# Optimization experiments

Measured on AMD Instinct MI355X. Metric: run time of the kernel, lower is better.

The kernel has to match this reference:

```python
import jax, jax.numpy as jnp
import numpy as np

RADIUS = 1.3
COARSE = 64
FINE = 2
N_ATOMS = 64
SH_DIM = 9
DATA_DIM = SH_DIM * 3 + 1  # 28
N_INTRS = COARSE * 3 * 2 * FINE  # 768
STEP = (RADIUS * 2.0 / COARSE / FINE) / 2.0
BATCH = 1024


def sh_basis(d):
    # real spherical harmonics basis, degree 2 (9 coeffs), on normalized dirs
    d = d / jnp.linalg.norm(d, axis=-1, keepdims=True)
    x, y, z = d[..., 0], d[..., 1], d[..., 2]
    C0 = 0.28209479177387814
    C1 = 0.4886025119029199
    C20, C21, C22, C23, C24 = (1.0925484305920792, -1.0925484305920792,
                               0.31539156525252005, -1.0925484305920792,
                               0.5462742152960396)
    return jnp.stack([
        C0 * jnp.ones_like(x), -C1 * y, C1 * z, -C1 * x,
        C20 * x * y, C21 * y * z, C22 * (2.0 * z * z - x * x - y * y),
        C23 * x * z, C24 * (x * x - y * y)
    ], axis=-1)


def dict_interp(grid, atoms, pts):
    # l2_interp_v2: coarse-voxel dictionary coeffs x trilinear fine-atom interp
    # pts: [P,3] in [0,1)
    P = pts.shape[0]
    pc = pts * COARSE
    c = jnp.clip(jnp.floor(pc), 0, COARSE - 1).astype(jnp.int32)
    local = pc - c.astype(pts.dtype)  # position inside coarse voxel, [0,1)
    clin = (c[:, 0] * COARSE + c[:, 1]) * COARSE + c[:, 2]
    coeff = grid[clin]                              # [P, A]
    # project dictionary coeffs through atoms for every fine cell: [P, FINE^3, D]
    proj = jnp.einsum('pa,fad->pfd', coeff, atoms)
    u = local * FINE - 0.5
    f = jnp.floor(u)
    t = u - f
    i0 = jnp.clip(f, 0, FINE - 1).astype(jnp.int32)
    i1 = jnp.clip(f + 1.0, 0, FINE - 1).astype(jnp.int32)
    idx = jnp.stack([i0, i1], axis=-1)              # [P,3,2]
    w = jnp.stack([1.0 - t, t], axis=-1)            # [P,3,2]
    rows = jnp.arange(P)
    out = jnp.zeros((P, DATA_DIM), dtype=pts.dtype)
    for kx in (0, 1):
        for ky in (0, 1):
            for kz in (0, 1):
                lin = (idx[:, 0, kx] * FINE + idx[:, 1, ky]) * FINE + idx[:, 2, kz]
                wgt = w[:, 0, kx] * w[:, 1, ky] * w[:, 2, kz]
                out = out + wgt[:, None] * proj[rows, lin]
    return out


def _forward(rays_o, rays_d, grid, atoms):
    dt = rays_o.dtype
    # ---- sample_proposal (no grad) ----
    off_pos = (RADIUS - rays_o) / rays_d
    off_neg = (-RADIUS - rays_o) / rays_d
    start = jnp.max(jnp.minimum(off_pos, off_neg), axis=-1, keepdims=True)
    intersections = jax.lax.stop_gradient(
        start + jnp.arange(N_INTRS, dtype=dt)[None, :] * STEP)  # [B, 768]
    tr = intersections[:, :-1]  # [B, 767]
    pts = rays_o[:, None, :] + tr[..., None] * rays_d[:, None, :]  # [B,n,3]
    mask = jnp.all((pts > -RADIUS) & (pts < RADIUS), axis=-1)      # [B,n]
    pts = jax.lax.stop_gradient(pts)
    B, n = tr.shape
    # normalized coords in [0,1); masked-out points are clipped then zeroed later
    p = jnp.clip((pts + RADIUS) / (2.0 * RADIUS), 0.0, 1.0 - 1e-6).reshape(-1, 3)
    data = dict_interp(grid, atoms, p).reshape(B, n, DATA_DIM)
    # masked_scatter of sigma <=> dense compute + where(mask, ., 0)
    sigma = jnp.where(mask, jax.nn.relu(data[..., -1]), 0.0)
    dists = (intersections[:, 1:] - intersections[:, :-1]) * \
        jnp.linalg.norm(rays_d, axis=-1, keepdims=True)
    alpha = 1.0 - jnp.exp(-sigma * dists)
    trans = jnp.cumprod(1.0 - alpha + 1e-10, axis=-1)
    trans = jnp.concatenate([jnp.ones_like(trans[:, :1]), trans[:, :-1]], axis=-1)
    abs_light = alpha * trans  # per-sample weights
    sh_mult = sh_basis(rays_d)                      # [B, 9]
    sh = data[..., :-1].reshape(B, n, 3, SH_DIM)
    rgb_samp = jnp.einsum('bnck,bk->bnc', sh, sh_mult)
    rgb_samp = jax.nn.sigmoid(jnp.where(mask[..., None], rgb_samp, 0.0))
    comp = jnp.sum(abs_light[..., None] * rgb_samp, axis=1)  # [B,3]
    acc = jnp.sum(abs_light, axis=1)
    rgb = comp + (1.0 - acc)[:, None]  # white background
    depth = jnp.sum(abs_light * tr, axis=1)
    return rgb, alpha, depth


def setup_inputs():
    key = jax.random.key(0)
    k0, k1, k2, k3 = jax.random.split(key, 4)
    o = jax.random.normal(k0, (BATCH, 3), dtype=jnp.float32)
    o = o / jnp.linalg.norm(o, axis=-1, keepdims=True) * 2.5
    d = -o + 0.3 * jax.random.normal(k1, (BATCH, 3), dtype=jnp.float32)
    d = d / jnp.linalg.norm(d, axis=-1, keepdims=True)
    grid = 0.01 * jax.random.normal(k2, (COARSE ** 3, N_ATOMS), dtype=jnp.float32)
    atoms_sh = jax.random.uniform(k3, (FINE ** 3, N_ATOMS, DATA_DIM - 1), dtype=jnp.float32)
    atoms = jnp.concatenate(
        [atoms_sh, jnp.full((FINE ** 3, N_ATOMS, 1), 0.01, dtype=jnp.float32)], axis=-1)
    return {"rays_o": o, "rays_d": d, "grid": grid, "atoms": atoms, "grid_id": 0}


def reference(rays_o, rays_d, grid, atoms, grid_id):
    # grid_id selects among num_scenes grids; num_scenes=1 so grid is pre-selected
    return _forward(rays_o, rays_d, grid, atoms)
```

## Files before the change

kernel.cpp:

```cpp
#include <hip/hip_runtime.h>
#include <hip/hip_bf16.h>

#define RADIUS_F 1.3f
#define NSAMP 767
#define STEPF 0.01015625f
#define BATCH 1024

typedef __attribute__((ext_vector_type(8))) short short8;
typedef __attribute__((ext_vector_type(4))) float floatx4;
typedef __fp16 fp16x2 __attribute__((ext_vector_type(2)));

static __device__ __forceinline__ unsigned pkbf(float a, float b) {
    union { __hip_bfloat162 h; unsigned u; } cvt;
    cvt.h = __float22bfloat162_rn(make_float2(a, b));
    return cvt.u;
}
static __device__ __forceinline__ unsigned pkh(float a, float b) {
    union { fp16x2 h; unsigned u; } c;
    c.h = __builtin_amdgcn_cvt_pkrtz(a, b);
    return c.u;
}
static __device__ __forceinline__ float2 uph(unsigned u) {
    union { unsigned u; fp16x2 h; } c; c.u = u;
    return make_float2((float)c.h.x, (float)c.h.y);
}
static __device__ __forceinline__ float bfx(unsigned short u) {
    union { unsigned u; float f; } c; c.u = ((unsigned)u) << 16; return c.f;
}

static __device__ __forceinline__ float coset4_sum(float p) {
    int q4 = __builtin_amdgcn_update_dpp(0, __float_as_int(p), 0x124, 0xf, 0xf, true);
    p = p + __int_as_float(q4);
    int q8 = __builtin_amdgcn_update_dpp(0, __float_as_int(p), 0x128, 0xf, 0xf, true);
    return p + __int_as_float(q8);
}

__launch_bounds__(512, 8)
__global__ void plenoxels_fwd(const float* __restrict__ rays_o,
                              const float* __restrict__ rays_d,
                              const float* __restrict__ grid,
                              const float* __restrict__ atoms,
                              float* __restrict__ out)
{
    __shared__ __align__(16) __hip_bfloat16 BpL[32 * 64];
    __shared__ unsigned WpU[768 * 5];
    __shared__ __align__(16) __hip_bfloat16 pL[768 * 4];
    __shared__ float wprodL[8];
    __shared__ float partL[8][5];

    const int tid  = threadIdx.x;
    const int ray  = blockIdx.x;
    const int lane = tid & 63;
    const int w    = tid >> 6;
    const int m    = lane & 15;
    const int quad = lane >> 4;

    const float ox = rays_o[ray * 3 + 0], oy = rays_o[ray * 3 + 1], oz = rays_o[ray * 3 + 2];
    const float dx = rays_d[ray * 3 + 0], dy = rays_d[ray * 3 + 1], dz = rays_d[ray * 3 + 2];

    float start;
    {
        float a0 = (RADIUS_F - ox) / dx, b0 = (-RADIUS_F - ox) / dx;
        float a1 = (RADIUS_F - oy) / dy, b1 = (-RADIUS_F - oy) / dy;
        float a2 = (RADIUS_F - oz) / dz, b2 = (-RADIUS_F - oz) / dz;
        start = fmaxf(fminf(a0, b0), fmaxf(fminf(a1, b1), fminf(a2, b2)));
    }
    const float dnorm = sqrtf(dx * dx + dy * dy + dz * dz);
    const float dist = STEPF * dnorm;

    auto geom = [&](int s) -> int {
        float tr = start + (float)s * STEPF;
        float px = ox + tr * dx, py = oy + tr * dy, pz = oz + tr * dz;
        int mask = (px > -RADIUS_F) & (px < RADIUS_F) &
                   (py > -RADIUS_F) & (py < RADIUS_F) &
                   (pz > -RADIUS_F) & (pz < RADIUS_F) & (s < NSAMP);
        float maskf = mask ? 1.f : 0.f;
        const float sc = 1.0f / (2.0f * RADIUS_F);
        float qx = fminf(fmaxf((px + RADIUS_F) * sc, 0.f), 1.0f - 1e-6f);
        float qy = fminf(fmaxf((py + RADIUS_F) * sc, 0.f), 1.0f - 1e-6f);
        float qz = fminf(fmaxf((pz + RADIUS_F) * sc, 0.f), 1.0f - 1e-6f);
        float pcx = qx * 64.f, pcy = qy * 64.f, pcz = qz * 64.f;
        float cx = fminf(floorf(pcx), 63.f);
        float cy = fminf(floorf(pcy), 63.f);
        float cz = fminf(floorf(pcz), 63.f);
        float lx = pcx - cx, ly = pcy - cy, lz = pcz - cz;
        int clin = (((int)cx * 64) + (int)cy) * 64 + (int)cz;
        float xw0, xw1, yw0, yw1, zw0, zw1;
        {
            float u = lx * 2.f - 0.5f, fF = floorf(u), t = u - fF;
            xw0 = (fF < 0.f) ? 1.f : ((fF > 0.f) ? 0.f : 1.f - t);
            xw1 = (fF < 0.f) ? 0.f : ((fF > 0.f) ? 1.f : t);
        }
        {
            float u = ly * 2.f - 0.5f, fF = floorf(u), t = u - fF;
            yw0 = (fF < 0.f) ? 1.f : ((fF > 0.f) ? 0.f : 1.f - t);
            yw1 = (fF < 0.f) ? 0.f : ((fF > 0.f) ? 1.f : t);
        }
        {
            float u = lz * 2.f - 0.5f, fF = floorf(u), t = u - fF;
            zw0 = (fF < 0.f) ? 1.f : ((fF > 0.f) ? 0.f : 1.f - t);
            zw1 = (fF < 0.f) ? 0.f : ((fF > 0.f) ? 1.f : t);
        }
        xw0 *= maskf; xw1 *= maskf;
        float g0 = yw0 * zw0, g1 = yw0 * zw1, g2 = yw1 * zw0, g3 = yw1 * zw1;
        unsigned* wr = &WpU[s * 5];
        wr[0] = pkh(xw0 * g0, xw1 * g0);
        wr[1] = pkh(xw0 * g1, xw1 * g1);
        wr[2] = pkh(xw0 * g2, xw1 * g2);
        wr[3] = pkh(xw0 * g3, xw1 * g3);
        return clin;
    };

    int clinA = geom(w * 96 + lane);
    int clinB = 0;
    if (lane < 32) clinB = geom(w * 96 + 64 + lane);

    const float4* g4 = (const float4*)grid;
    float4 cv0, cv1, cv2, cv3;
    {
        int clinC = __shfl(clinA, m, 64);
        const float4* gp = g4 + (clinC << 4) + (quad << 2);
        cv0 = gp[0]; cv1 = gp[1]; cv2 = gp[2]; cv3 = gp[3];
    }

    {
        float shm[9];
        float inv = 1.0f / dnorm;
        float nx = dx * inv, ny = dy * inv, nz = dz * inv;
        shm[0] = 0.28209479177387814f;
        shm[1] = -0.4886025119029199f * ny;
        shm[2] = 0.4886025119029199f * nz;
        shm[3] = -0.4886025119029199f * nx;
        shm[4] = 1.0925484305920792f * nx * ny;
        shm[5] = -1.0925484305920792f * ny * nz;
        shm[6] = 0.31539156525252005f * (2.f * nz * nz - nx * nx - ny * ny);
        shm[7] = -1.0925484305920792f * nx * nz;
        shm[8] = 0.5462742152960396f * (nx * nx - ny * ny);

        const float* base = atoms + tid * 28;
        float4 v0 = *(const float4*)(base);
        float4 v1 = *(const float4*)(base + 4);
        float4 v2 = *(const float4*)(base + 8);
        float4 v3 = *(const float4*)(base + 12);
        float4 v4 = *(const float4*)(base + 16);
        float4 v5 = *(const float4*)(base + 20);
        float4 v6 = *(const float4*)(base + 24);

        float s0 = v0.x*shm[0] + v0.y*shm[1] + v0.z*shm[2] + v0.w*shm[3]
                 + v1.x*shm[4] + v1.y*shm[5] + v1.z*shm[6] + v1.w*shm[7] + v2.x*shm[8];
        float s1 = v2.y*shm[0] + v2.z*shm[1] + v2.w*shm[2] + v3.x*shm[3]
                 + v3.y*shm[4] + v3.z*shm[5] + v3.w*shm[6] + v4.x*shm[7] + v4.y*shm[8];
        float s2 = v4.z*shm[0] + v4.w*shm[1] + v5.x*shm[2] + v5.y*shm[3]
                 + v5.z*shm[4] + v5.w*shm[5] + v6.x*shm[6] + v6.y*shm[7] + v6.z*shm[8];

        int f = tid >> 6, a = tid & 63;
        int cb = (f << 2) << 6;
        BpL[cb + a]        = __float2bfloat16(s0);
        BpL[cb + 64 + a]   = __float2bfloat16(s1);
        BpL[cb + 128 + a]  = __float2bfloat16(s2);
        BpL[cb + 192 + a]  = __float2bfloat16(v6.w);
    }
    __syncthreads();

    short8 bq00, bq01, bq10, bq11;
    {
        const short* bs = (const short*)BpL;
        const short* p0 = bs + m * 64 + (quad << 4);
        bq00 = *(const short8*)(p0);
        bq01 = *(const short8*)(p0 + 8);
        const short* p1 = bs + (16 + m) * 64 + (quad << 4);
        bq10 = *(const short8*)(p1);
        bq11 = *(const short8*)(p1 + 8);
    }

    float* out_rgb   = out;
    float* out_alpha = out + BATCH * 3;
    float* out_depth = out + BATCH * 3 + BATCH * NSAMP;
    const int f0 = m >> 2;

    #pragma unroll
    for (int t = 0; t < 6; ++t) {
        union { unsigned u[4]; short8 s; } a0, a1;
        a0.u[0] = pkbf(cv0.x, cv0.y); a0.u[1] = pkbf(cv0.z, cv0.w);
        a0.u[2] = pkbf(cv1.x, cv1.y); a0.u[3] = pkbf(cv1.z, cv1.w);
        a1.u[0] = pkbf(cv2.x, cv2.y); a1.u[1] = pkbf(cv2.z, cv2.w);
        a1.u[2] = pkbf(cv3.x, cv3.y); a1.u[3] = pkbf(cv3.z, cv3.w);

        if (t < 5) {
            int tn = t + 1;
            int clinC = (tn < 4) ? __shfl(clinA, (tn << 4) + m, 64)
                                 : __shfl(clinB, ((tn - 4) << 4) + m, 64);
            const float4* gp = g4 + (clinC << 4) + (quad << 2);
            cv0 = gp[0]; cv1 = gp[1]; cv2 = gp[2]; cv3 = gp[3];
        }

        floatx4 acc0 = {0.f, 0.f, 0.f, 0.f};
        floatx4 acc1 = {0.f, 0.f, 0.f, 0.f};
        acc0 = __builtin_amdgcn_mfma_f32_16x16x32_bf16(a0.s, bq00, acc0, 0, 0, 0);
        acc0 = __builtin_amdgcn_mfma_f32_16x16x32_bf16(a1.s, bq01, acc0, 0, 0, 0);
        acc1 = __builtin_amdgcn_mfma_f32_16x16x32_bf16(a0.s, bq10, acc1, 0, 0, 0);
        acc1 = __builtin_amdgcn_mfma_f32_16x16x32_bf16(a1.s, bq11, acc1, 0, 0, 0);

        #pragma unroll
        for (int r = 0; r < 4; ++r) {
            int s = w * 96 + (t << 4) + (quad << 2) + r;
            float2 wab = uph(WpU[s * 5 + f0]);
            float p = wab.x * acc0[r] + wab.y * acc1[r];
            p = coset4_sum(p);
            if (m < 4) pL[(s << 2) + m] = __float2bfloat16(p);
        }
    }

    __syncthreads();

    {
        const bool act = (tid < 384);
        const int s0 = tid * 2;
        float a0 = 0.f, a1 = 0.f;
        float r0 = 0.f, g0 = 0.f, b0 = 0.f, r1 = 0.f, g1 = 0.f, b1 = 0.f;
        if (act) {
            short8 pv = *(const short8*)&pL[s0 << 2];
            a0 = 1.f - __expf(-fmaxf(bfx((unsigned short)pv[3]), 0.f) * dist);
            a1 = 1.f - __expf(-fmaxf(bfx((unsigned short)pv[7]), 0.f) * dist);
            r0 = 1.f / (1.f + __expf(-bfx((unsigned short)pv[0])));
            g0 = 1.f / (1.f + __expf(-bfx((unsigned short)pv[1])));
            b0 = 1.f / (1.f + __expf(-bfx((unsigned short)pv[2])));
            r1 = 1.f / (1.f + __expf(-bfx((unsigned short)pv[4])));
            g1 = 1.f / (1.f + __expf(-bfx((unsigned short)pv[5])));
            b1 = 1.f / (1.f + __expf(-bfx((unsigned short)pv[6])));
            out_alpha[ray * NSAMP + s0] = a0;
            if (s0 + 1 < NSAMP) out_alpha[ray * NSAMP + s0 + 1] = a1;
        }
        float pr = (1.f - a0 + 1e-10f) * (1.f - a1 + 1e-10f);

        float incl = pr;
        #pragma unroll
        for (int off = 1; off < 64; off <<= 1) {
            float v = __shfl_up(incl, off, 64);
            if (lane >= off) incl *= v;
        }
        if (lane == 63) wprodL[w] = incl;
        __syncthreads();

        float base = 1.f;
        #pragma unroll
        for (int ww = 0; ww < 5; ++ww)
            if (w > ww) base *= wprodL[ww];
        float excl = __shfl_up(incl, 1, 64);
        if (lane == 0) excl = 1.f;
        float trans = base * excl;

        float c0 = 0.f, c1 = 0.f, c2 = 0.f, accw = 0.f, dep = 0.f;
        if (act) {
            float w0 = a0 * trans;
            c0 += w0 * r0; c1 += w0 * g0; c2 += w0 * b0;
            accw += w0;
            dep += w0 * (start + (float)s0 * STEPF);
            trans *= (1.f - a0 + 1e-10f);
            float w1 = a1 * trans;
            c0 += w1 * r1; c1 += w1 * g1; c2 += w1 * b1;
            accw += w1;
            dep += w1 * (start + (float)(s0 + 1) * STEPF);
        }
        #pragma unroll
        for (int off = 1; off < 64; off <<= 1) {
            c0   += __shfl_xor(c0, off, 64);
            c1   += __shfl_xor(c1, off, 64);
            c2   += __shfl_xor(c2, off, 64);
            accw += __shfl_xor(accw, off, 64);
            dep  += __shfl_xor(dep, off, 64);
        }
        if (lane == 0) {
            partL[w][0] = c0; partL[w][1] = c1; partL[w][2] = c2;
            partL[w][3] = accw; partL[w][4] = dep;
        }
        __syncthreads();
        if (tid == 0) {
            float C0 = 0.f, C1 = 0.f, C2 = 0.f, AC = 0.f, DP = 0.f;
            #pragma unroll
            for (int ww = 0; ww < 6; ++ww) {
                C0 += partL[ww][0]; C1 += partL[ww][1]; C2 += partL[ww][2];
                AC += partL[ww][3]; DP += partL[ww][4];
            }
            float bg = 1.f - AC;
            out_rgb[ray * 3 + 0] = C0 + bg;
            out_rgb[ray * 3 + 1] = C1 + bg;
            out_rgb[ray * 3 + 2] = C2 + bg;
            out_depth[ray] = DP;
        }
    }
}

extern "C" void kernel_launch(void* const* d_in, const int* in_sizes, int n_in,
                              void* d_out, int out_size, void* d_ws, size_t ws_size,
                              hipStream_t stream) {
    const float* rays_o = (const float*)d_in[0];
    const float* rays_d = (const float*)d_in[1];
    const float* grid   = (const float*)d_in[2];
    const float* atoms  = (const float*)d_in[3];
    float* out = (float*)d_out;
    hipLaunchKernelGGL(plenoxels_fwd, dim3(BATCH), dim3(512), 0, stream,
                       rays_o, rays_d, grid, atoms, out);
}
```

Measured before the change: 114.3 us.

## Skip samples outside the box and fuse activations into the MFMA epilogue

Computes each ray's box exit time and the number of samples that can be inside the box. It then distributes only those samples across the waves, so grid gathers and MFMA tiles run only for that range. Samples beyond the range are written as zero alpha, which matches the masked reference. Sigmoid and alpha activations move into the MFMA epilogue and are stored as fp32. Interpolation weights get a transposed layout for vector loads, and the B staging buffer is padded to reduce LDS bank conflicts. In exchange, the unrolled fixed loop becomes a runtime-bounded one, and the trip count varies across blocks.

```diff
diff --git a/kernel.cpp b/kernel.cpp
--- a/kernel.cpp
+++ b/kernel.cpp
@@ -8,6 +8,7 @@
 
 typedef __attribute__((ext_vector_type(8))) short short8;
 typedef __attribute__((ext_vector_type(4))) float floatx4;
+typedef __attribute__((ext_vector_type(4))) unsigned uintx4;
 typedef __fp16 fp16x2 __attribute__((ext_vector_type(2)));
 
 static __device__ __forceinline__ unsigned pkbf(float a, float b) {
@@ -23,9 +24,6 @@
 static __device__ __forceinline__ float2 uph(unsigned u) {
     union { unsigned u; fp16x2 h; } c; c.u = u;
     return make_float2((float)c.h.x, (float)c.h.y);
-}
-static __device__ __forceinline__ float bfx(unsigned short u) {
-    union { unsigned u; float f; } c; c.u = ((unsigned)u) << 16; return c.f;
 }
 
 static __device__ __forceinline__ float coset4_sum(float p) {
@@ -42,9 +40,9 @@
                               const float* __restrict__ atoms,
                               float* __restrict__ out)
 {
-    __shared__ __align__(16) __hip_bfloat16 BpL[32 * 64];
-    __shared__ unsigned WpU[768 * 5];
-    __shared__ __align__(16) __hip_bfloat16 pL[768 * 4];
+    __shared__ __align__(16) __hip_bfloat16 BpL[32 * 72];
+    __shared__ __align__(16) unsigned WtU[4 * 776];
+    __shared__ __align__(16) float pAct[768 * 4];
     __shared__ float wprodL[8];
     __shared__ float partL[8][5];
 
@@ -58,15 +56,25 @@
     const float ox = rays_o[ray * 3 + 0], oy = rays_o[ray * 3 + 1], oz = rays_o[ray * 3 + 2];
     const float dx = rays_d[ray * 3 + 0], dy = rays_d[ray * 3 + 1], dz = rays_d[ray * 3 + 2];
 
-    float start;
+    float start, exitT;
     {
         float a0 = (RADIUS_F - ox) / dx, b0 = (-RADIUS_F - ox) / dx;
         float a1 = (RADIUS_F - oy) / dy, b1 = (-RADIUS_F - oy) / dy;
         float a2 = (RADIUS_F - oz) / dz, b2 = (-RADIUS_F - oz) / dz;
         start = fmaxf(fminf(a0, b0), fmaxf(fminf(a1, b1), fminf(a2, b2)));
+        exitT = fminf(fmaxf(a0, b0), fminf(fmaxf(a1, b1), fmaxf(a2, b2)));
     }
     const float dnorm = sqrtf(dx * dx + dy * dy + dz * dz);
     const float dist = STEPF * dnorm;
+
+    int nAct;
+    {
+        float span = (exitT - start) / STEPF;
+        if (span >= 0.f) nAct = (span < 765.f) ? ((int)span + 2) : NSAMP;
+        else             nAct = (span < 0.f) ? 0 : NSAMP;
+    }
+    const int seg = ((nAct + 127) >> 7) << 4;
+    const int nT  = seg >> 4;
 
     auto geom = [&](int s) -> int {
         float tr = start + (float)s * STEPF;
@@ -103,21 +111,20 @@
         }
         xw0 *= maskf; xw1 *= maskf;
         float g0 = yw0 * zw0, g1 = yw0 * zw1, g2 = yw1 * zw0, g3 = yw1 * zw1;
-        unsigned* wr = &WpU[s * 5];
-        wr[0] = pkh(xw0 * g0, xw1 * g0);
-        wr[1] = pkh(xw0 * g1, xw1 * g1);
-        wr[2] = pkh(xw0 * g2, xw1 * g2);
-        wr[3] = pkh(xw0 * g3, xw1 * g3);
+        WtU[       s] = pkh(xw0 * g0, xw1 * g0);
+        WtU[ 776 + s] = pkh(xw0 * g1, xw1 * g1);
+        WtU[1552 + s] = pkh(xw0 * g2, xw1 * g2);
+        WtU[2328 + s] = pkh(xw0 * g3, xw1 * g3);
         return clin;
     };
 
-    int clinA = geom(w * 96 + lane);
-    int clinB = 0;
-    if (lane < 32) clinB = geom(w * 96 + 64 + lane);
+    int clinA = 0, clinB = 0;
+    if (lane < seg)      clinA = geom(w * seg + lane);
+    if (lane + 64 < seg) clinB = geom(w * seg + 64 + lane);
 
     const float4* g4 = (const float4*)grid;
     float4 cv0, cv1, cv2, cv3;
-    {
+    if (nT > 0) {
         int clinC = __shfl(clinA, m, 64);
         const float4* gp = g4 + (clinC << 4) + (quad << 2);
         cv0 = gp[0]; cv1 = gp[1]; cv2 = gp[2]; cv3 = gp[3];
@@ -154,21 +161,21 @@
                  + v5.z*shm[4] + v5.w*shm[5] + v6.x*shm[6] + v6.y*shm[7] + v6.z*shm[8];
 
         int f = tid >> 6, a = tid & 63;
-        int cb = (f << 2) << 6;
-        BpL[cb + a]        = __float2bfloat16(s0);
-        BpL[cb + 64 + a]   = __float2bfloat16(s1);
-        BpL[cb + 128 + a]  = __float2bfloat16(s2);
-        BpL[cb + 192 + a]  = __float2bfloat16(v6.w);
+        int cb = (f << 2) * 72 + a;
+        BpL[cb]        = __float2bfloat16(s0);
+        BpL[cb + 72]   = __float2bfloat16(s1);
+        BpL[cb + 144]  = __float2bfloat16(s2);
+        BpL[cb + 216]  = __float2bfloat16(v6.w);
     }
     __syncthreads();
 
     short8 bq00, bq01, bq10, bq11;
     {
         const short* bs = (const short*)BpL;
-        const short* p0 = bs + m * 64 + (quad << 4);
+        const short* p0 = bs + m * 72 + (quad << 4);
         bq00 = *(const short8*)(p0);
         bq01 = *(const short8*)(p0 + 8);
-        const short* p1 = bs + (16 + m) * 64 + (quad << 4);
+        const short* p1 = bs + (16 + m) * 72 + (quad << 4);
         bq10 = *(const short8*)(p1);
         bq11 = *(const short8*)(p1 + 8);
     }
@@ -178,56 +185,61 @@
     float* out_depth = out + BATCH * 3 + BATCH * NSAMP;
     const int f0 = m >> 2;
 
-    #pragma unroll
-    for (int t = 0; t < 6; ++t) {
-        union { unsigned u[4]; short8 s; } a0, a1;
-        a0.u[0] = pkbf(cv0.x, cv0.y); a0.u[1] = pkbf(cv0.z, cv0.w);
-        a0.u[2] = pkbf(cv1.x, cv1.y); a0.u[3] = pkbf(cv1.z, cv1.w);
-        a1.u[0] = pkbf(cv2.x, cv2.y); a1.u[1] = pkbf(cv2.z, cv2.w);
-        a1.u[2] = pkbf(cv3.x, cv3.y); a1.u[3] = pkbf(cv3.z, cv3.w);
-
-        if (t < 5) {
-            int tn = t + 1;
-            int clinC = (tn < 4) ? __shfl(clinA, (tn << 4) + m, 64)
-                                 : __shfl(clinB, ((tn - 4) << 4) + m, 64);
+    for (int t = 0; t < nT; ++t) {
+        union { unsigned u[4]; short8 s; } a0p, a1p;
+        a0p.u[0] = pkbf(cv0.x, cv0.y); a0p.u[1] = pkbf(cv0.z, cv0.w);
+        a0p.u[2] = pkbf(cv1.x, cv1.y); a0p.u[3] = pkbf(cv1.z, cv1.w);
+        a1p.u[0] = pkbf(cv2.x, cv2.y); a1p.u[1] = pkbf(cv2.z, cv2.w);
+        a1p.u[2] = pkbf(cv3.x, cv3.y); a1p.u[3] = pkbf(cv3.z, cv3.w);
+
+        if (t + 1 < nT) {
+            int idx = ((t + 1) << 4) + m;
+            int clinC = (idx < 64) ? __shfl(clinA, idx, 64)
+                                   : __shfl(clinB, idx - 64, 64);
             const float4* gp = g4 + (clinC << 4) + (quad << 2);
             cv0 = gp[0]; cv1 = gp[1]; cv2 = gp[2]; cv3 = gp[3];
         }
 
         floatx4 acc0 = {0.f, 0.f, 0.f, 0.f};
         floatx4 acc1 = {0.f, 0.f, 0.f, 0.f};
-        acc0 = __builtin_amdgcn_mfma_f32_16x16x32_bf16(a0.s, bq00, acc0, 0, 0, 0);
-        acc0 = __builtin_amdgcn_mfma_f32_16x16x32_bf16(a1.s, bq01, acc0, 0, 0, 0);
-        acc1 = __builtin_amdgcn_mfma_f32_16x16x32_bf16(a0.s, bq10, acc1, 0, 0, 0);
-        acc1 = __builtin_amdgcn_mfma_f32_16x16x32_bf16(a1.s, bq11, acc1, 0, 0, 0);
-
+        acc0 = __builtin_amdgcn_mfma_f32_16x16x32_bf16(a0p.s, bq00, acc0, 0, 0, 0);
+        acc0 = __builtin_amdgcn_mfma_f32_16x16x32_bf16(a1p.s, bq01, acc0, 0, 0, 0);
+        acc1 = __builtin_amdgcn_mfma_f32_16x16x32_bf16(a0p.s, bq10, acc1, 0, 0, 0);
+        acc1 = __builtin_amdgcn_mfma_f32_16x16x32_bf16(a1p.s, bq11, acc1, 0, 0, 0);
+
+        int sb = w * seg + (t << 4) + (quad << 2);
+        union { uintx4 v; unsigned u[4]; } wt;
+        wt.v = *(const uintx4*)&WtU[f0 * 776 + sb];
         #pragma unroll
         for (int r = 0; r < 4; ++r) {
-            int s = w * 96 + (t << 4) + (quad << 2) + r;
-            float2 wab = uph(WpU[s * 5 + f0]);
+            float2 wab = uph(wt.u[r]);
             float p = wab.x * acc0[r] + wab.y * acc1[r];
             p = coset4_sum(p);
-            if (m < 4) pL[(s << 2) + m] = __float2bfloat16(p);
+            if (m < 4) {
+                float e = __expf((m == 3) ? (-fmaxf(p, 0.f) * dist) : -p);
+                float v = (m == 3) ? (1.f - e) : (1.f / (1.f + e));
+                pAct[((sb + r) << 2) + m] = v;
+            }
         }
     }
 
     __syncthreads();
 
     {
+        const int sLim = seg << 3;
         const bool act = (tid < 384);
         const int s0 = tid * 2;
         float a0 = 0.f, a1 = 0.f;
-        float r0 = 0.f, g0 = 0.f, b0 = 0.f, r1 = 0.f, g1 = 0.f, b1 = 0.f;
+        float r0 = 0.f, g0c = 0.f, b0c = 0.f, r1 = 0.f, g1c = 0.f, b1c = 0.f;
         if (act) {
-            short8 pv = *(const short8*)&pL[s0 << 2];
-            a0 = 1.f - __expf(-fmaxf(bfx((unsigned short)pv[3]), 0.f) * dist);
-            a1 = 1.f - __expf(-fmaxf(bfx((unsigned short)pv[7]), 0.f) * dist);
-            r0 = 1.f / (1.f + __expf(-bfx((unsigned short)pv[0])));
-            g0 = 1.f / (1.f + __expf(-bfx((unsigned short)pv[1])));
-            b0 = 1.f / (1.f + __expf(-bfx((unsigned short)pv[2])));
-            r1 = 1.f / (1.f + __expf(-bfx((unsigned short)pv[4])));
-            g1 = 1.f / (1.f + __expf(-bfx((unsigned short)pv[5])));
-            b1 = 1.f / (1.f + __expf(-bfx((unsigned short)pv[6])));
+            if (s0 < sLim) {
+                float4 q = *(const float4*)&pAct[s0 << 2];
+                r0 = q.x; g0c = q.y; b0c = q.z; a0 = q.w;
+            }
+            if (s0 + 1 < sLim) {
+                float4 q = *(const float4*)&pAct[(s0 + 1) << 2];
+                r1 = q.x; g1c = q.y; b1c = q.z; a1 = q.w;
+            }
             out_alpha[ray * NSAMP + s0] = a0;
             if (s0 + 1 < NSAMP) out_alpha[ray * NSAMP + s0 + 1] = a1;
         }
@@ -253,12 +265,12 @@
         float c0 = 0.f, c1 = 0.f, c2 = 0.f, accw = 0.f, dep = 0.f;
         if (act) {
             float w0 = a0 * trans;
-            c0 += w0 * r0; c1 += w0 * g0; c2 += w0 * b0;
+            c0 += w0 * r0; c1 += w0 * g0c; c2 += w0 * b0c;
             accw += w0;
             dep += w0 * (start + (float)s0 * STEPF);
             trans *= (1.f - a0 + 1e-10f);
             float w1 = a1 * trans;
-            c0 += w1 * r1; c1 += w1 * g1; c2 += w1 * b1;
+            c0 += w1 * r1; c1 += w1 * g1c; c2 += w1 * b1c;
             accw += w1;
             dep += w1 * (start + (float)(s0 + 1) * STEPF);
         }
```

Result: slower. 129.4 us (+13.2%).
